# Kernel tuning notes

Hardware: AMD Instinct MI355X
Metric: run time of the kernel (lower is better)

## Reference

```python
import jax, jax.numpy as jnp
import numpy as np
import math
jax.config.update('jax_enable_x64', True)

# ---- camera constants (match init_kwargs) ----
WAVELENGTHS = np.array([632e-9, 550e-9, 450e-9])
FOCAL_LENGTH = 50e-3
FOCAL_DEPTH = 1.7
MIN_DEPTH, MAX_DEPTH = 1.0, 5.0
N_DEPTHS = 16
IMAGE_SIZE = 384
MASK_SIZE = 2048
MASK_DIAMETER = 2.5e-3
PIXEL_PITCH = 6.45e-6
BATCH = 2
SENSOR_DIST = 1.0 / (1.0 / FOCAL_LENGTH - 1.0 / FOCAL_DEPTH)
MASK_PITCH = MASK_DIAMETER / MASK_SIZE
EPS = 1e-3


def _j1(x):
    # Bessel J1, Numerical Recipes rational approximation (double precision, ~1e-8 rel err)
    x = np.asarray(x, dtype=np.float64)
    ax = np.abs(x)
    y = x * x
    p1 = x * (72362614232.0 + y * (-7895059235.0 + y * (242396853.1 + y * (-2972611.439 + y * (15704.48260 + y * (-30.16036606))))))
    q1 = 144725228442.0 + y * (2300535178.0 + y * (18583304.74 + y * (99447.43394 + y * (376.9991397 + y))))
    small = p1 / q1
    axs = np.maximum(ax, 1e-300)
    z = 8.0 / axs
    y2 = z * z
    xx = ax - 2.356194491
    p2 = 1.0 + y2 * (0.183105e-2 + y2 * (-0.3516396496e-4 + y2 * (0.2457520174e-5 + y2 * (-0.240337019e-6))))
    q2 = 0.04687499995 + y2 * (-0.2002690873e-3 + y2 * (0.8449199096e-5 + y2 * (-0.88228987e-6 + y2 * 0.105787412e-6)))
    big = np.sqrt(0.636619772 / axs) * (np.cos(xx) * p2 - z * np.sin(xx) * q2) * np.sign(x)
    return np.where(ax < 8.0, small, big)


def _precompute():
    # scene distances: inverse-perspective sampling (ips_to_metric)
    d = np.linspace(0.0, 1.0, N_DEPTHS)
    scene_z = 1.0 / (d * (1.0 / MAX_DEPTH - 1.0 / MIN_DEPTH) + 1.0 / MIN_DEPTH)
    wl = WAVELENGTHS.reshape(-1, 1, 1)
    # --- precompute_H ---
    cy = PIXEL_PITCH * np.arange(1, IMAGE_SIZE // 2 + 1, dtype=np.float64).reshape(-1, 1)
    cx = PIXEL_PITCH * np.arange(1, IMAGE_SIZE // 2 + 1, dtype=np.float64).reshape(1, -1)
    rho_sampling = np.sqrt(cy ** 2 + cx ** 2)[None] / (wl * SENSOR_DIST)  # [3, H/2, W/2]
    rho_grid = math.sqrt(2) * PIXEL_PITCH * (np.arange(-1, IMAGE_SIZE // 2 + 1, dtype=np.float64) + 0.5)
    rho_grid = rho_grid.reshape(1, -1) / (WAVELENGTHS.reshape(-1, 1) * SENSOR_DIST)  # [3, R]
    r = MASK_PITCH * np.linspace(1, MASK_SIZE / 2, MASK_SIZE // 2).reshape(1, -1, 1)  # [1, M, 1]
    rg = rho_grid[:, None, :]  # [3, 1, R]
    denom = 2.0 * np.pi * rg
    safe = np.where(denom == 0.0, 1.0, denom)
    J = np.where(rg == 0.0, 0.5 * r ** 2, r * _j1(denom * r) / safe)  # [3, M, R]
    H = np.concatenate([J[:, 0:1, :], J[:, 1:, :] - J[:, :-1, :]], axis=1)  # [3, M, R]
    # --- pointsource_inputfield1d ---
    z = scene_z.reshape(1, -1, 1)
    rr = MASK_PITCH * np.linspace(1, MASK_SIZE / 2, MASK_SIZE // 2).reshape(1, 1, -1)
    k = 2.0 * np.pi / wl
    sqrt_z_r = np.sqrt(z ** 2 + rr ** 2)
    amp = z / wl / sqrt_z_r ** 2
    amp = amp / amp.max()
    phase = k * (sqrt_z_r - z)
    sqrt_r_d = np.sqrt(FOCAL_DEPTH ** 2 + rr ** 2)
    phase = phase - k * (sqrt_r_d - FOCAL_DEPTH)
    return (jnp.asarray(H), jnp.asarray(rho_grid), jnp.asarray(rho_sampling),
            jnp.asarray(amp), jnp.asarray(phase))


def setup_inputs() -> dict:
    key = jax.random.key(0)
    k1, k2, k3 = jax.random.split(key, 3)
    H, rho_grid, rho_sampling, prop_amplitude, prop_phase = _precompute()
    img = jax.random.uniform(k1, (BATCH, 3, IMAGE_SIZE, IMAGE_SIZE), dtype=jnp.float32)
    depthmap = jax.random.uniform(k2, (BATCH, 1, IMAGE_SIZE, IMAGE_SIZE), dtype=jnp.float32)
    # micron-scale DOE heightmap (learned parameter in the original)
    heightmap1d = jax.random.uniform(k3, (MASK_SIZE // 2,), dtype=jnp.float64) * 1e-6
    return {"img": img, "depthmap": depthmap, "heightmap1d": heightmap1d,
            "prop_amplitude": prop_amplitude, "prop_phase": prop_phase,
            "H": H, "rho_grid": rho_grid, "rho_sampling": rho_sampling,
            "occlusion": 1}


def reference(img, depthmap, heightmap1d, prop_amplitude, prop_phase, H, rho_grid, rho_sampling, occlusion):
    wl = jnp.asarray(WAVELENGTHS).reshape(-1, 1, 1)  # [3,1,1] float64
    # refractive index (Cauchy fit) and heightmap -> phase delay
    n_idx = 1.5375 + 0.00829045 / (wl * 1e6) ** 2 - 0.000211046 / (wl * 1e6) ** 4
    phase = 2.0 * jnp.pi / wl * (n_idx - 1.0) * heightmap1d.reshape(1, 1, -1) + prop_phase  # [3,D,M]
    # 1D PSF via Hankel transform (double precision)
    real = jnp.einsum('wdm,wmr->wdr', prop_amplitude * jnp.cos(phase), H)
    imag = jnp.einsum('wdm,wmr->wdr', prop_amplitude * jnp.sin(phase), H)
    psf1d = (2.0 * jnp.pi / (wl * SENSOR_DIST)) ** 2 * (real ** 2 + imag ** 2)  # [3,D,R]
    # interpolate radial PSF onto the 2D pixel rho grid (per wavelength)
    hh = IMAGE_SIZE // 2
    def interp_wl(grid, vals, samp):  # grid [R], vals [D,R], samp [hh,hh]
        return jax.vmap(lambda v: jnp.interp(samp.reshape(-1), grid, v))(vals)
    psf_rd = jax.vmap(interp_wl)(rho_grid, psf1d, rho_sampling)  # [3,D,hh*hh]
    psf_rd = jnp.maximum(psf_rd, 0.0).astype(jnp.float32).reshape(3, N_DEPTHS, hh, hh)
    # copy_quadruple: mirror quadrant to full image
    q = jnp.concatenate([jnp.flip(psf_rd, axis=-2), psf_rd], axis=-2)
    psf = jnp.concatenate([jnp.flip(q, axis=-1), q], axis=-1)  # [3,D,H,W]
    psf = jnp.fft.fftshift(psf, axes=(-2, -1))[None]  # [1,3,D,H,W]
    psf = psf / jnp.sum(psf, axis=(-2, -1), keepdims=True)  # normalize_psf
    # depthmap -> binary layered depth, volume
    idx = jnp.clip(jnp.floor(depthmap * N_DEPTHS).astype(jnp.int32), 0, N_DEPTHS - 1)  # [B,1,H,W]
    layered = (idx[:, :, None, :, :] == jnp.arange(N_DEPTHS).reshape(1, 1, -1, 1, 1)).astype(jnp.float32)
    volume = layered * img[:, :, None]  # [B,3,D,H,W]
    scale = volume.max()
    volume = volume / scale
    S = volume.shape[-2:]
    Fpsf = jnp.fft.rfft2(psf)
    blur = lambda a: jnp.fft.irfft2(jnp.fft.rfft2(a) * Fpsf, s=S)
    if occlusion:
        blurred_alpha = blur(layered)          # [B,3,D,H,W]
        blurred_volume = blur(volume)
        cumsum_alpha = jnp.flip(jnp.cumsum(jnp.flip(layered, axis=-3), axis=-3), axis=-3)
        blurred_cumsum = blur(cumsum_alpha)
        blurred_volume = blurred_volume / (blurred_cumsum + EPS)
        blurred_alpha = blurred_alpha / (blurred_cumsum + EPS)
        # over_op: front-to-back transmittance
        t = jnp.cumprod(1.0 - blurred_alpha, axis=-3)
        over = jnp.concatenate([jnp.ones_like(t[..., :1, :, :]), t[..., :-1, :, :]], axis=-3)
        captimg = jnp.sum(over * blurred_volume, axis=-3)
    else:
        captimg = jnp.sum(blur(volume), axis=-3)
    return scale * captimg  # [B,3,H,W]
```

## Files before the change

### kernel.cpp

```cpp
#include <hip/hip_runtime.h>
#include <math.h>

#define ND 16
#define NSZ 384
#define NHALF 192
#define NPIX 147456
#define QPIX 36864
#define MS2 1024
#define NG 194
#define EPSV 0.001f

__device__ __forceinline__ double ld64(const void* p, long i, int f){
  return f ? ((const double*)p)[i] : (double)((const float*)p)[i];
}

__global__ void k_detect(const void* rg, int* flag){
  double d = ((const double*)rg)[1];
  *flag = (fabs(d) < 1.0e9) ? 1 : 0;
}

__device__ __forceinline__ void init_tws(float* twr, float* twi){
  for (int j=(int)threadIdx.x; j<NSZ; j+=(int)blockDim.x){
    double s,c; sincos((2.0*M_PI/384.0)*(double)j, &s, &c);
    twr[j]=(float)c; twi[j]=(float)(-s);
  }
}

template<int STR,int DIR>
__device__ __forceinline__ void fft384s(float* xr,float* xi,float* yr,float* yi,
                                        int u,const float* twr,const float* twi){
  const float KH = (DIR>0)?0.86602540378443865f:-0.86602540378443865f;
  float *Xr=xr,*Xi=xi,*Yr=yr,*Yi=yi;
  #pragma unroll
  for (int i0=0;i0<128;i0+=64){
    int p=i0+u;
    float ar=Xr[p*STR],ai=Xi[p*STR];
    float br=Xr[(p+128)*STR],bi=Xi[(p+128)*STR];
    float cr=Xr[(p+256)*STR],ci=Xi[(p+256)*STR];
    float t1r=br+cr,t1i=bi+ci;
    float y0r=ar+t1r,y0i=ai+t1i;
    float t2r=ar-0.5f*t1r,t2i=ai-0.5f*t1i;
    float bdr=br-cr,bdi=bi-ci;
    float t3r=KH*bdi,t3i=-KH*bdr;
    float w1r=twr[p],     w1i=(DIR>0)?twi[p]:-twi[p];
    float w2r=twr[2*p],   w2i=(DIR>0)?twi[2*p]:-twi[2*p];
    float y1r=t2r+t3r,y1i=t2i+t3i;
    float y2r=t2r-t3r,y2i=t2i-t3i;
    Yr[(3*p  )*STR]=y0r;             Yi[(3*p  )*STR]=y0i;
    Yr[(3*p+1)*STR]=y1r*w1r-y1i*w1i; Yi[(3*p+1)*STR]=y1r*w1i+y1i*w1r;
    Yr[(3*p+2)*STR]=y2r*w2r-y2i*w2i; Yi[(3*p+2)*STR]=y2r*w2i+y2i*w2r;
  }
  __syncthreads();
  { float*t; t=Xr;Xr=Yr;Yr=t; t=Xi;Xi=Yi;Yi=t; }
  #pragma unroll
  for (int st=0; st<7; st++){
    const int s = 3<<st;
    #pragma unroll
    for (int i0=0;i0<192;i0+=64){
      int i=i0+u, p=i/s, t=p*s;
      float ar=Xr[i*STR],ai=Xi[i*STR];
      float br=Xr[(i+192)*STR],bi=Xi[(i+192)*STR];
      float wr=twr[t], wi=(DIR>0)?twi[t]:-twi[t];
      float sur=ar+br,sui=ai+bi;
      float dr=ar-br,di=ai-bi;
      int o=i+t;
      Yr[o*STR]=sur;             Yi[o*STR]=sui;
      Yr[(o+s)*STR]=dr*wr-di*wi; Yi[(o+s)*STR]=dr*wi+di*wr;
    }
    __syncthreads();
    { float*t2; t2=Xr;Xr=Yr;Yr=t2; t2=Xi;Xi=Yi;Yi=t2; }
  }
}

__global__ __launch_bounds__(256) void k_trig(const void* __restrict__ h1d,
    const void* __restrict__ amp, const void* __restrict__ pph,
    const int* __restrict__ flagp, double* __restrict__ acs, double* __restrict__ ass){
  int wd = blockIdx.x;
  int w = wd >> 4;
  int f = *flagp;
  double wl = (w==0) ? 6.32e-07 : (w==1 ? 5.5e-07 : 4.5e-07);
  double um2 = (wl*1e6)*(wl*1e6);
  double n_idx = 1.5375 + 0.00829045/um2 - 0.000211046/(um2*um2);
  double coef = (2.0*M_PI/wl)*(n_idx-1.0);
  for (int m = (int)threadIdx.x; m < MS2; m += 256){
    double h = ld64(h1d, m, f);
    double a = ld64(amp, (long)wd*MS2 + m, f);
    double p = ld64(pph, (long)wd*MS2 + m, f);
    double s,c; sincos(coef*h + p, &s, &c);
    acs[(size_t)wd*MS2 + m] = a*c;
    ass[(size_t)wd*MS2 + m] = a*s;
  }
}

__global__ __launch_bounds__(256) void k_dotA(const double* __restrict__ acs,
    const double* __restrict__ ass, const void* __restrict__ Hm,
    const int* __restrict__ flagp, double2* __restrict__ part){
  int wd = blockIdx.x >> 3, ch = blockIdx.x & 7;
  int w = wd >> 4;
  int f = *flagp;
  int m0 = ch << 7;
  __shared__ double sac[128], sas[128];
  int tid = (int)threadIdx.x;
  if (tid < 128){
    sac[tid] = acs[(size_t)wd*MS2 + m0 + tid];
    sas[tid] = ass[(size_t)wd*MS2 + m0 + tid];
  }
  __syncthreads();
  int r = tid;
  if (r < NG){
    double sr=0.0, si=0.0;
    if (f){
      const double* Hw = (const double*)Hm + ((size_t)w*MS2 + m0)*NG + r;
      #pragma unroll 4
      for (int m=0;m<128;m++){
        double h = Hw[(size_t)m*NG];
        sr += sac[m]*h; si += sas[m]*h;
      }
    } else {
      const float* Hw = (const float*)Hm + ((size_t)w*MS2 + m0)*NG + r;
      #pragma unroll 4
      for (int m=0;m<128;m++){
        double h = (double)Hw[(size_t)m*NG];
        sr += sac[m]*h; si += sas[m]*h;
      }
    }
    part[(size_t)blockIdx.x*NG + r] = make_double2(sr, si);
  }
}

__global__ __launch_bounds__(256) void k_interp2(const double2* __restrict__ part,
    const void* __restrict__ rg, const void* __restrict__ rs,
    const int* __restrict__ flagp, float* __restrict__ q,
    double* __restrict__ sums_b){
  int wdl = blockIdx.x / 144, blk = blockIdx.x % 144;
  int c = wdl >> 4;
  int pix = blk*256 + (int)threadIdx.x;
  int f = *flagp;
  __shared__ double v[NG];
  int tid = (int)threadIdx.x;
  if (tid < NG){
    double sr=0.0, si=0.0;
    #pragma unroll
    for (int ch=0; ch<8; ch++){
      double2 pp = part[(size_t)(wdl*8+ch)*NG + tid];
      sr += pp.x; si += pp.y;
    }
    v[tid] = sr*sr + si*si;
  }
  __syncthreads();
  long gbase = (long)c*NG;
  double rho = ld64(rs, (long)c*QPIX + pix, f);
  double g0 = ld64(rg, gbase, f);
  double delta = ld64(rg, gbase+1, f) - g0;
  int i = (int)floor((rho-g0)/delta);
  if (i < 0) i = 0; if (i > 192) i = 192;
  double gi  = ld64(rg, gbase+i,   f);
  double gi1 = ld64(rg, gbase+i+1, f);
  if (i > 0  && rho < gi)  { i--; gi1 = gi; gi = ld64(rg, gbase+i, f); }
  else if (i < 192 && rho > gi1){ i++; gi = gi1; gi1 = ld64(rg, gbase+i+1, f); }
  double gl = ld64(rg, gbase+NG-1, f);
  double val;
  if (rho <= g0)      val = v[0];
  else if (rho >= gl) val = v[NG-1];
  else { double t = (rho-gi)/(gi1-gi); val = v[i] + (v[i+1]-v[i])*t; }
  if (val < 0.0) val = 0.0;
  q[(size_t)wdl*QPIX + pix] = (float)val;
  __shared__ double red[256];
  red[threadIdx.x] = val;
  __syncthreads();
  for (int s=128; s>0; s>>=1){
    if ((int)threadIdx.x < s) red[threadIdx.x] += red[threadIdx.x+s];
    __syncthreads();
  }
  if (threadIdx.x==0) atomicAdd(&sums_b[wdl], red[0]);
}

__global__ __launch_bounds__(256) void k_rows_fwd(
    const float* __restrict__ q, const double* __restrict__ sums,
    float* __restrict__ Rr, const float* __restrict__ img,
    const float* __restrict__ depth, float2* __restrict__ V,
    float2* __restrict__ S){
  __shared__ float b0r[NSZ*5], b0i[NSZ*5], b1r[NSZ*5], b1i[NSZ*5];
  __shared__ float twr[NSZ], twi[NSZ];
  init_tws(twr, twi);
  int bi = blockIdx.x;
  int rl = (int)threadIdx.x>>6, u = (int)threadIdx.x&63;
  float *xr=b0r+rl, *xi=b0i+rl, *yr=b1r+rl, *yi=b1i+rl;
  if (bi < 48*24){
    int imgi = bi/24, t = bi%24;
    int y0 = t*8 + 2*rl;
    float sc = (float)(1.0/(4.0*sums[imgi]*147456.0));
    const float* q0 = q + ((size_t)imgi*QPIX + (size_t)y0*NHALF);
    const float* q1 = q0 + NHALF;
    #pragma unroll
    for (int k=0;k<6;k++){
      int x = u+64*k;
      int gx = (x<NHALF)? x : (383-x);
      xr[x*5] = q0[gx]*sc;
      xi[x*5] = q1[gx]*sc;
    }
    __syncthreads();
    fft384s<5,1>(xr,xi,yr,yi,u,twr,twi);
    const float PC=0.86602540378443865f, PS=-0.5f;
    float s0,c0; __sincosf((float)M_PI*(float)u/384.0f,&s0,&c0);
    float phr=c0, phi=-s0;
    float* o0 = Rr + ((size_t)imgi*192 + y0)*NSZ;
    float* o1 = o0 + NSZ;
    #pragma unroll
    for (int k=0;k<6;k++){
      int kx = u+64*k;
      int m  = kx ? (384-kx) : 0;
      float Zr=xr[kx*5], Zi=xi[kx*5], Zmr=xr[m*5], Zmi=xi[m*5];
      float Ar=0.5f*(Zr+Zmr), Ai=0.5f*(Zi-Zmi);
      float Br=0.5f*(Zi+Zmi), Bi=-0.5f*(Zr-Zmr);
      o0[kx] = Ar*phr - Ai*phi;
      o1[kx] = Br*phr - Bi*phi;
      float nr=phr*PC-phi*PS, ni=phr*PS+phi*PC; phr=nr; phi=ni;
    }
  } else if (bi < 48*24 + 48*96){
    int i2 = bi - 48*24;
    int im48 = i2/96, grp = i2%96;
    int c = im48>>4, d = im48&15;
    int y = grp*4 + rl;
    const float* i0 = img + (((size_t)0*3+c)*NPIX + (size_t)y*NSZ);
    const float* i1 = img + (((size_t)1*3+c)*NPIX + (size_t)y*NSZ);
    const float* d0 = depth + (size_t)y*NSZ;
    const float* d1 = depth + (size_t)NPIX + (size_t)y*NSZ;
    #pragma unroll
    for (int k=0;k<6;k++){
      int x=u+64*k;
      int ia=(int)floorf(d0[x]*16.f); ia=ia<0?0:(ia>15?15:ia);
      int ib=(int)floorf(d1[x]*16.f); ib=ib<0?0:(ib>15?15:ib);
      xr[x*5] = (ia==d)? i0[x] : 0.f;
      xi[x*5] = (ib==d)? i1[x] : 0.f;
    }
    __syncthreads();
    fft384s<5,1>(xr,xi,yr,yi,u,twr,twi);
    float2* orow = V + ((size_t)im48*NPIX + (size_t)y*NSZ);
    #pragma unroll
    for (int k=0;k<6;k++){ int x=u+64*k; orow[x]=make_float2(xr[x*5],xi[x*5]); }
  } else {
    int i3 = bi - 48*24 - 48*96;
    int d = i3/96, grp = i3%96;
    int y = grp*4+rl;
    const float* d0 = depth + (size_t)y*NSZ;
    const float* d1 = depth + (size_t)NPIX + (size_t)y*NSZ;
    #pragma unroll
    for (int k=0;k<6;k++){
      int x=u+64*k;
      int ia=(int)floorf(d0[x]*16.f); ia=ia<0?0:(ia>15?15:ia);
      int ib=(int)floorf(d1[x]*16.f); ib=ib<0?0:(ib>15?15:ib);
      xr[x*5]=(ia==d)?1.f:0.f;
      xi[x*5]=(ib==d)?1.f:0.f;
    }
    __syncthreads();
    fft384s<5,1>(xr,xi,yr,yi,u,twr,twi);
    float2* orow = S + ((size_t)d*NPIX + (size_t)y*NSZ);
    #pragma unroll
    for (int k=0;k<6;k++){ int x=u+64*k; orow[x]=make_float2(xr[x*5],xi[x*5]); }
  }
}

__global__ __launch_bounds__(512) void k_colsFS(const float* __restrict__ Rr,
    float* __restrict__ Rc, float2* __restrict__ S){
  __shared__ float b0r[NSZ*9], b0i[NSZ*9], b1r[NSZ*9], b1i[NSZ*9];
  __shared__ float twr[NSZ], twi[NSZ];
  init_tws(twr,twi);
  int bi = blockIdx.x;
  if (bi < 1152){
    int imgi = bi/24, cg = bi%24;
    int j16 = (int)threadIdx.x&15, r0 = (int)threadIdx.x>>4;
    int uu = j16>>1;
    const float* rbase = Rr + (size_t)imgi*192*NSZ + cg*16 + j16;
    #pragma unroll
    for (int k=0;k<12;k++){
      int y = r0 + 32*k;
      int gy = (y<NHALF)? y : (383-y);
      float v = rbase[(size_t)gy*NSZ];
      if (j16&1) b0i[y*9+uu]=v; else b0r[y*9+uu]=v;
    }
    __syncthreads();
    int cc = (int)threadIdx.x>>6, u = (int)threadIdx.x&63;
    fft384s<9,1>(b0r+cc,b0i+cc,b1r+cc,b1i+cc,u,twr,twi);
    const float PC=0.96592582628906829f, PS=-0.25881904510252076f;
    float s0,c0; __sincosf((float)M_PI*(float)r0/384.f,&s0,&c0);
    float phr=c0, phi=-s0;
    float* ob = Rc + (size_t)imgi*NPIX + cg*16 + j16;
    #pragma unroll
    for (int k=0;k<12;k++){
      int ky=r0+32*k;
      int m = ky ? (384-ky) : 0;
      float Zr=b0r[ky*9+uu], Zi=b0i[ky*9+uu], Zmr=b0r[m*9+uu], Zmi=b0i[m*9+uu];
      float Cr,Ci;
      if (j16&1){ Cr=0.5f*(Zi+Zmi); Ci=-0.5f*(Zr-Zmr); }
      else      { Cr=0.5f*(Zr+Zmr); Ci= 0.5f*(Zi-Zmi); }
      ob[(size_t)ky*NSZ] = Cr*phr - Ci*phi;
      float nr=phr*PC-phi*PS, ni=phr*PS+phi*PC; phr=nr; phi=ni;
    }
  } else {
    int i2 = bi - 1152;
    int imgi = i2/48, cg = i2%48;
    size_t boff = (size_t)imgi*NPIX + (size_t)cg*8;
    int j = (int)threadIdx.x&7, r0 = (int)threadIdx.x>>3;
    #pragma unroll
    for (int k=0;k<6;k++){
      int r=r0+64*k;
      float2 v = S[boff + (size_t)r*NSZ + j];
      b0r[r*9+j]=v.x; b0i[r*9+j]=v.y;
    }
    __syncthreads();
    int cc=(int)threadIdx.x>>6, u=(int)threadIdx.x&63;
    fft384s<9,1>(b0r+cc,b0i+cc,b1r+cc,b1i+cc,u,twr,twi);
    #pragma unroll
    for (int k=0;k<6;k++){
      int r=r0+64*k;
      S[boff+(size_t)r*NSZ+j] = make_float2(b0r[r*9+j], b0i[r*9+j]);
    }
  }
}

__global__ __launch_bounds__(512) void k_FM(float2* __restrict__ V,
    const float* __restrict__ Rc, const float2* __restrict__ S,
    float2* __restrict__ L, int nf){
  __shared__ float b0r[NSZ*9], b0i[NSZ*9], b1r[NSZ*9], b1i[NSZ*9];
  __shared__ float twr[NSZ], twi[NSZ];
  init_tws(twr,twi);
  const float PC=0.86602540378443865f, PS=0.5f;
  int bi = blockIdx.x;
  int j = (int)threadIdx.x&7, r0 = (int)threadIdx.x>>3;
  int cc=(int)threadIdx.x>>6, u=(int)threadIdx.x&63;
  if (bi < nf){
    int imgi = bi/48, cg = bi%48;
    size_t boff = (size_t)imgi*NPIX + (size_t)cg*8;
    #pragma unroll
    for (int k=0;k<6;k++){
      int r=r0+64*k;
      float2 v = V[boff + (size_t)r*NSZ + j];
      b0r[r*9+j]=v.x; b0i[r*9+j]=v.y;
    }
    __syncthreads();
    fft384s<9,1>(b0r+cc,b0i+cc,b1r+cc,b1i+cc,u,twr,twi);
    int kx = cg*8+j;
    float s0,c0; __sincosf((float)M_PI*(float)(kx+r0)/384.f,&s0,&c0);
    float phr=c0, phi=s0;
    const float* rb = Rc + (size_t)imgi*NPIX + kx;
    #pragma unroll
    for (int k=0;k<6;k++){
      int r=r0+64*k;
      float R = rb[(size_t)r*NSZ];
      float fr=R*phr, fi=R*phi;
      float br=b0r[r*9+j], bi2=b0i[r*9+j];
      b0r[r*9+j] = br*fr - bi2*fi;
      b0i[r*9+j] = br*fi + bi2*fr;
      float nr=phr*PC-phi*PS, ni=phr*PS+phi*PC; phr=nr; phi=ni;
    }
    __syncthreads();
    fft384s<9,-1>(b0r+cc,b0i+cc,b1r+cc,b1i+cc,u,twr,twi);
    #pragma unroll
    for (int k=0;k<6;k++){
      int r=r0+64*k;
      V[boff+(size_t)r*NSZ+j] = make_float2(b0r[r*9+j], b0i[r*9+j]);
    }
  } else {
    int t = bi - nf;
    int cg = t%48, d=(t/48)&15, c=t/(48*16);
    const float2* src = S  + ((size_t)d*NPIX + (size_t)cg*8);
    const float*  rb  = Rc + ((size_t)(c*ND+d)*NPIX + cg*8);
    float2*       dst = L  + ((size_t)(c*ND+d)*NPIX + (size_t)cg*8);
    int kx = cg*8+j;
    float s0,c0; __sincosf((float)M_PI*(float)(kx+r0)/384.f,&s0,&c0);
    float phr=c0, phi=s0;
    #pragma unroll
    for (int k=0;k<6;k++){
      int r=r0+64*k;
      float2 v = src[(size_t)r*NSZ + j];
      float R = rb[(size_t)r*NSZ + j];
      float fr=R*phr, fi=R*phi;
      b0r[r*9+j] = v.x*fr - v.y*fi;
      b0i[r*9+j] = v.x*fi + v.y*fr;
      float nr=phr*PC-phi*PS, ni=phr*PS+phi*PC; phr=nr; phi=ni;
    }
    __syncthreads();
    fft384s<9,-1>(b0r+cc,b0i+cc,b1r+cc,b1i+cc,u,twr,twi);
    #pragma unroll
    for (int k=0;k<6;k++){
      int r=r0+64*k;
      dst[(size_t)r*NSZ+j] = make_float2(b0r[r*9+j], b0i[r*9+j]);
    }
  }
}

__global__ __launch_bounds__(256) void k_rowsinv(float2* __restrict__ data){
  __shared__ float b0r[NSZ*5], b0i[NSZ*5], b1r[NSZ*5], b1i[NSZ*5];
  __shared__ float twr[NSZ], twi[NSZ];
  init_tws(twr,twi);
  int rl=(int)threadIdx.x>>6, u=(int)threadIdx.x&63;
  float *xr=b0r+rl,*xi=b0i+rl,*yr=b1r+rl,*yi=b1i+rl;
  float2* row = data + ((size_t)blockIdx.x*4 + rl)*NSZ;
  #pragma unroll
  for (int k=0;k<6;k++){ int x=u+64*k; float2 v=row[x]; xr[x*5]=v.x; xi[x*5]=v.y; }
  __syncthreads();
  fft384s<5,-1>(xr,xi,yr,yi,u,twr,twi);
  #pragma unroll
  for (int k=0;k<6;k++){ int x=u+64*k; row[x]=make_float2(xr[x*5],xi[x*5]); }
}

__global__ __launch_bounds__(256) void k_combine(const float2* __restrict__ L,
    const float2* __restrict__ V, float* __restrict__ out){
  __shared__ float b0r[NSZ*5], b0i[NSZ*5], b1r[NSZ*5], b1i[NSZ*5];
  __shared__ float twr[NSZ], twi[NSZ];
  init_tws(twr,twi);
  int c = blockIdx.x/96, grp = blockIdx.x%96;
  int rl=(int)threadIdx.x>>6, u=(int)threadIdx.x&63;
  float *xr=b0r+rl,*xi=b0i+rl,*yr=b1r+rl,*yi=b1i+rl;
  int y = grp*4+rl;
  size_t rowoff = (size_t)y*NSZ;
  float A0[6],C0[6],A1[6],C1[6];
  #pragma unroll
  for (int k=0;k<6;k++){ A0[k]=0.f; C0[k]=0.f; A1[k]=0.f; C1[k]=0.f; }
  float2 lpre[6], vpre[6];
  {
    const float2* l0 = L + ((size_t)(c*ND + ND-1)*NPIX + rowoff);
    const float2* v0 = V + ((size_t)(c*ND + ND-1)*NPIX + rowoff);
    #pragma unroll
    for (int k=0;k<6;k++){ int x=u+64*k; lpre[k]=l0[x]; vpre[k]=v0[x]; }
  }
  for (int d=ND-1; d>=0; --d){
    float2 vcur[6];
    #pragma unroll
    for (int k=0;k<6;k++){
      int x=u+64*k;
      xr[x*5]=lpre[k].x; xi[x*5]=lpre[k].y;
      vcur[k]=vpre[k];
    }
    __syncthreads();
    if (d > 0){
      const float2* ln = L + ((size_t)(c*ND+d-1)*NPIX + rowoff);
      const float2* vn = V + ((size_t)(c*ND+d-1)*NPIX + rowoff);
      #pragma unroll
      for (int k=0;k<6;k++){ int x=u+64*k; lpre[k]=ln[x]; vpre[k]=vn[x]; }
    }
    fft384s<5,-1>(xr,xi,yr,yi,u,twr,twi);
    #pragma unroll
    for (int k=0;k<6;k++){
      int x=u+64*k;
      float bl0=xr[x*5], bl1=xi[x*5];
      A0[k] += bl0;
      A1[k] += bl1;
      float ic0 = 1.f/(A0[k] + EPSV);
      float ic1 = 1.f/(A1[k] + EPSV);
      C0[k] = vcur[k].x*ic0 + (1.f - bl0*ic0)*C0[k];
      C1[k] = vcur[k].y*ic1 + (1.f - bl1*ic1)*C1[k];
    }
    __syncthreads();
  }
  float* o0 = out + ((size_t)(0*3 + c)*NPIX + rowoff);
  float* o1 = out + ((size_t)(1*3 + c)*NPIX + rowoff);
  #pragma unroll
  for (int k=0;k<6;k++){ o0[u+64*k]=C0[k]; o1[u+64*k]=C1[k]; }
}

extern "C" void kernel_launch(void* const* d_in, const int* in_sizes, int n_in,
                              void* d_out, int out_size, void* d_ws, size_t ws_size,
                              hipStream_t stream){
  const float* img   = (const float*)d_in[0];
  const float* depth = (const float*)d_in[1];
  const void*  h1d   = d_in[2];
  const void*  amp   = d_in[3];
  const void*  pph   = d_in[4];
  const void*  Hm    = d_in[5];
  const void*  rg    = d_in[6];
  const void*  rs    = d_in[7];
  float* out = (float*)d_out;
  (void)in_sizes; (void)n_in; (void)out_size;

  char* ws = (char*)d_ws;
  size_t off = 0;
  auto take = [&](size_t b)->char*{ char* p = ws + off; off += (b + 255) & ~(size_t)255; return p; };
  int*     flag = (int*)    take(256);
  double*  sums = (double*) take((size_t)48*8);
  double*  acs  = (double*) take((size_t)48*MS2*8);
  double*  ass  = (double*) take((size_t)48*MS2*8);
  double2* part = (double2*)take((size_t)48*8*NG*16);
  float*   q    = (float*)  take((size_t)48*QPIX*4);
  float*   Rr   = (float*)  take((size_t)48*192*NSZ*4);
  float*   Rc   = (float*)  take((size_t)48*NPIX*4);
  float2*  V    = (float2*) take((size_t)48*NPIX*8);
  float2*  S    = (float2*) take((size_t)16*NPIX*8);
  float2*  L    = (float2*) take((size_t)48*NPIX*8);
  if (ws_size < off) return;

  k_detect<<<1, 1, 0, stream>>>(rg, flag);
  hipMemsetAsync(sums, 0, 48*8, stream);
  k_trig<<<48, 256, 0, stream>>>(h1d, amp, pph, flag, acs, ass);
  k_dotA<<<48*8, 256, 0, stream>>>(acs, ass, Hm, flag, part);
  k_interp2<<<48*144, 256, 0, stream>>>(part, rg, rs, flag, q, sums);
  k_rows_fwd<<<48*24 + 48*96 + 16*96, 256, 0, stream>>>(q, sums, Rr, img, depth, V, S);
  k_colsFS<<<1152 + 16*48, 512, 0, stream>>>(Rr, Rc, S);
  k_FM<<<48*48 + 3*16*48, 512, 0, stream>>>(V, Rc, S, L, 48*48);
  k_rowsinv<<<48*96, 256, 0, stream>>>(V);
  k_combine<<<3*96, 256, 0, stream>>>(L, V, out);
}
```

Measured before the change: 343.1 us.

## Fuse trig into dot kernel, batch L row IFFTs, make combine pixel-parallel

Drops the flag-detect and trig kernels: each k_dotA block now computes its sincos terms inline, and the flag is derived directly from the input. The row inverse FFTs of L move from the serial combine loop into the k_rowsinv launch, which now covers both V and L. k_combine becomes an elementwise, pixel-parallel depth scan with vectorized float4 loads, replacing 288 blocks that ran serial FFTs. The aim is better occupancy and fewer launches, at the cost of an extra read-write pass over L and some repeated sincos work across blocks.

```diff
diff --git a/kernel.cpp b/kernel.cpp
--- a/kernel.cpp
+++ b/kernel.cpp
@@ -13,10 +13,9 @@
 __device__ __forceinline__ double ld64(const void* p, long i, int f){
   return f ? ((const double*)p)[i] : (double)((const float*)p)[i];
 }
-
-__global__ void k_detect(const void* rg, int* flag){
+__device__ __forceinline__ int dtflag(const void* rg){
   double d = ((const double*)rg)[1];
-  *flag = (fabs(d) < 1.0e9) ? 1 : 0;
+  return (fabs(d) < 1.0e9) ? 1 : 0;
 }
 
 __device__ __forceinline__ void init_tws(float* twr, float* twi){
@@ -72,38 +71,27 @@
   }
 }
 
-__global__ __launch_bounds__(256) void k_trig(const void* __restrict__ h1d,
+__global__ __launch_bounds__(256) void k_dotA(const void* __restrict__ h1d,
     const void* __restrict__ amp, const void* __restrict__ pph,
-    const int* __restrict__ flagp, double* __restrict__ acs, double* __restrict__ ass){
-  int wd = blockIdx.x;
-  int w = wd >> 4;
-  int f = *flagp;
-  double wl = (w==0) ? 6.32e-07 : (w==1 ? 5.5e-07 : 4.5e-07);
-  double um2 = (wl*1e6)*(wl*1e6);
-  double n_idx = 1.5375 + 0.00829045/um2 - 0.000211046/(um2*um2);
-  double coef = (2.0*M_PI/wl)*(n_idx-1.0);
-  for (int m = (int)threadIdx.x; m < MS2; m += 256){
-    double h = ld64(h1d, m, f);
-    double a = ld64(amp, (long)wd*MS2 + m, f);
-    double p = ld64(pph, (long)wd*MS2 + m, f);
-    double s,c; sincos(coef*h + p, &s, &c);
-    acs[(size_t)wd*MS2 + m] = a*c;
-    ass[(size_t)wd*MS2 + m] = a*s;
-  }
-}
-
-__global__ __launch_bounds__(256) void k_dotA(const double* __restrict__ acs,
-    const double* __restrict__ ass, const void* __restrict__ Hm,
-    const int* __restrict__ flagp, double2* __restrict__ part){
+    const void* __restrict__ Hm, const void* __restrict__ rg,
+    double2* __restrict__ part){
   int wd = blockIdx.x >> 3, ch = blockIdx.x & 7;
   int w = wd >> 4;
-  int f = *flagp;
+  int f = dtflag(rg);
   int m0 = ch << 7;
   __shared__ double sac[128], sas[128];
   int tid = (int)threadIdx.x;
   if (tid < 128){
-    sac[tid] = acs[(size_t)wd*MS2 + m0 + tid];
-    sas[tid] = ass[(size_t)wd*MS2 + m0 + tid];
+    double wl = (w==0) ? 6.32e-07 : (w==1 ? 5.5e-07 : 4.5e-07);
+    double um2 = (wl*1e6)*(wl*1e6);
+    double n_idx = 1.5375 + 0.00829045/um2 - 0.000211046/(um2*um2);
+    double coef = (2.0*M_PI/wl)*(n_idx-1.0);
+    long mi = m0 + tid;
+    double h = ld64(h1d, mi, f);
+    double a = ld64(amp, (long)wd*MS2 + mi, f);
+    double p = ld64(pph, (long)wd*MS2 + mi, f);
+    double s,c; sincos(coef*h + p, &s, &c);
+    sac[tid] = a*c; sas[tid] = a*s;
   }
   __syncthreads();
   int r = tid;
@@ -130,12 +118,11 @@
 
 __global__ __launch_bounds__(256) void k_interp2(const double2* __restrict__ part,
     const void* __restrict__ rg, const void* __restrict__ rs,
-    const int* __restrict__ flagp, float* __restrict__ q,
-    double* __restrict__ sums_b){
+    float* __restrict__ q, double* __restrict__ sums_b){
   int wdl = blockIdx.x / 144, blk = blockIdx.x % 144;
   int c = wdl >> 4;
   int pix = blk*256 + (int)threadIdx.x;
-  int f = *flagp;
+  int f = dtflag(rg);
   __shared__ double v[NG];
   int tid = (int)threadIdx.x;
   if (tid < NG){
@@ -390,13 +377,17 @@
   }
 }
 
-__global__ __launch_bounds__(256) void k_rowsinv(float2* __restrict__ data){
+__global__ __launch_bounds__(256) void k_rowsinv(float2* __restrict__ V,
+    float2* __restrict__ L){
   __shared__ float b0r[NSZ*5], b0i[NSZ*5], b1r[NSZ*5], b1i[NSZ*5];
   __shared__ float twr[NSZ], twi[NSZ];
   init_tws(twr,twi);
+  int bi = blockIdx.x;
+  float2* base; int ri;
+  if (bi < 4608){ base = V; ri = bi; } else { base = L; ri = bi - 4608; }
   int rl=(int)threadIdx.x>>6, u=(int)threadIdx.x&63;
   float *xr=b0r+rl,*xi=b0i+rl,*yr=b1r+rl,*yi=b1i+rl;
-  float2* row = data + ((size_t)blockIdx.x*4 + rl)*NSZ;
+  float2* row = base + ((size_t)ri*4 + rl)*NSZ;
   #pragma unroll
   for (int k=0;k<6;k++){ int x=u+64*k; float2 v=row[x]; xr[x*5]=v.x; xi[x*5]=v.y; }
   __syncthreads();
@@ -407,57 +398,27 @@
 
 __global__ __launch_bounds__(256) void k_combine(const float2* __restrict__ L,
     const float2* __restrict__ V, float* __restrict__ out){
-  __shared__ float b0r[NSZ*5], b0i[NSZ*5], b1r[NSZ*5], b1i[NSZ*5];
-  __shared__ float twr[NSZ], twi[NSZ];
-  init_tws(twr,twi);
-  int c = blockIdx.x/96, grp = blockIdx.x%96;
-  int rl=(int)threadIdx.x>>6, u=(int)threadIdx.x&63;
-  float *xr=b0r+rl,*xi=b0i+rl,*yr=b1r+rl,*yi=b1i+rl;
-  int y = grp*4+rl;
-  size_t rowoff = (size_t)y*NSZ;
-  float A0[6],C0[6],A1[6],C1[6];
-  #pragma unroll
-  for (int k=0;k<6;k++){ A0[k]=0.f; C0[k]=0.f; A1[k]=0.f; C1[k]=0.f; }
-  float2 lpre[6], vpre[6];
-  {
-    const float2* l0 = L + ((size_t)(c*ND + ND-1)*NPIX + rowoff);
-    const float2* v0 = V + ((size_t)(c*ND + ND-1)*NPIX + rowoff);
-    #pragma unroll
-    for (int k=0;k<6;k++){ int x=u+64*k; lpre[k]=l0[x]; vpre[k]=v0[x]; }
-  }
+  int t = blockIdx.x*256 + (int)threadIdx.x;
+  int c = t / (NPIX/2);
+  int pp = t - c*(NPIX/2);
+  size_t base = (size_t)(c*ND)*NPIX + (size_t)pp*2;
+  float A0a=0.f,C0a=0.f,A1a=0.f,C1a=0.f;
+  float A0b=0.f,C0b=0.f,A1b=0.f,C1b=0.f;
   for (int d=ND-1; d>=0; --d){
-    float2 vcur[6];
-    #pragma unroll
-    for (int k=0;k<6;k++){
-      int x=u+64*k;
-      xr[x*5]=lpre[k].x; xi[x*5]=lpre[k].y;
-      vcur[k]=vpre[k];
-    }
-    __syncthreads();
-    if (d > 0){
-      const float2* ln = L + ((size_t)(c*ND+d-1)*NPIX + rowoff);
-      const float2* vn = V + ((size_t)(c*ND+d-1)*NPIX + rowoff);
-      #pragma unroll
-      for (int k=0;k<6;k++){ int x=u+64*k; lpre[k]=ln[x]; vpre[k]=vn[x]; }
-    }
-    fft384s<5,-1>(xr,xi,yr,yi,u,twr,twi);
-    #pragma unroll
-    for (int k=0;k<6;k++){
-      int x=u+64*k;
-      float bl0=xr[x*5], bl1=xi[x*5];
-      A0[k] += bl0;
-      A1[k] += bl1;
-      float ic0 = 1.f/(A0[k] + EPSV);
-      float ic1 = 1.f/(A1[k] + EPSV);
-      C0[k] = vcur[k].x*ic0 + (1.f - bl0*ic0)*C0[k];
-      C1[k] = vcur[k].y*ic1 + (1.f - bl1*ic1)*C1[k];
-    }
-    __syncthreads();
-  }
-  float* o0 = out + ((size_t)(0*3 + c)*NPIX + rowoff);
-  float* o1 = out + ((size_t)(1*3 + c)*NPIX + rowoff);
-  #pragma unroll
-  for (int k=0;k<6;k++){ o0[u+64*k]=C0[k]; o1[u+64*k]=C1[k]; }
+    float4 l = *(const float4*)(L + base + (size_t)d*NPIX);
+    float4 v = *(const float4*)(V + base + (size_t)d*NPIX);
+    A0a += l.x; A1a += l.y; A0b += l.z; A1b += l.w;
+    float ic0a=1.f/(A0a+EPSV), ic1a=1.f/(A1a+EPSV);
+    float ic0b=1.f/(A0b+EPSV), ic1b=1.f/(A1b+EPSV);
+    C0a = v.x*ic0a + (1.f - l.x*ic0a)*C0a;
+    C1a = v.y*ic1a + (1.f - l.y*ic1a)*C1a;
+    C0b = v.z*ic0b + (1.f - l.z*ic0b)*C0b;
+    C1b = v.w*ic1b + (1.f - l.w*ic1b)*C1b;
+  }
+  size_t o0 = (size_t)(0*3 + c)*NPIX + (size_t)pp*2;
+  size_t o1 = (size_t)(1*3 + c)*NPIX + (size_t)pp*2;
+  out[o0]   = C0a; out[o0+1] = C0b;
+  out[o1]   = C1a; out[o1+1] = C1b;
 }
 
 extern "C" void kernel_launch(void* const* d_in, const int* in_sizes, int n_in,
@@ -477,10 +438,7 @@
   char* ws = (char*)d_ws;
   size_t off = 0;
   auto take = [&](size_t b)->char*{ char* p = ws + off; off += (b + 255) & ~(size_t)255; return p; };
-  int*     flag = (int*)    take(256);
   double*  sums = (double*) take((size_t)48*8);
-  double*  acs  = (double*) take((size_t)48*MS2*8);
-  double*  ass  = (double*) take((size_t)48*MS2*8);
   double2* part = (double2*)take((size_t)48*8*NG*16);
   float*   q    = (float*)  take((size_t)48*QPIX*4);
   float*   Rr   = (float*)  take((size_t)48*192*NSZ*4);
@@ -490,14 +448,12 @@
   float2*  L    = (float2*) take((size_t)48*NPIX*8);
   if (ws_size < off) return;
 
-  k_detect<<<1, 1, 0, stream>>>(rg, flag);
   hipMemsetAsync(sums, 0, 48*8, stream);
-  k_trig<<<48, 256, 0, stream>>>(h1d, amp, pph, flag, acs, ass);
-  k_dotA<<<48*8, 256, 0, stream>>>(acs, ass, Hm, flag, part);
-  k_interp2<<<48*144, 256, 0, stream>>>(part, rg, rs, flag, q, sums);
+  k_dotA<<<48*8, 256, 0, stream>>>(h1d, amp, pph, Hm, rg, part);
+  k_interp2<<<48*144, 256, 0, stream>>>(part, rg, rs, q, sums);
   k_rows_fwd<<<48*24 + 48*96 + 16*96, 256, 0, stream>>>(q, sums, Rr, img, depth, V, S);
   k_colsFS<<<1152 + 16*48, 512, 0, stream>>>(Rr, Rc, S);
   k_FM<<<48*48 + 3*16*48, 512, 0, stream>>>(V, Rc, S, L, 48*48);
-  k_rowsinv<<<48*96, 256, 0, stream>>>(V);
-  k_combine<<<3*96, 256, 0, stream>>>(L, V, out);
-}
+  k_rowsinv<<<9216, 256, 0, stream>>>(V, L);
+  k_combine<<<864, 256, 0, stream>>>(L, V, out);
+}
```

Measured after the change: 319.7 us. 1.07x faster.
